# Optimization experiments

Measured on AMD Instinct MI355X. Metric: run time of the kernel, lower is better.

Reference implementation:

```python
import jax, jax.numpy as jnp
import numpy as np

B, S, HID = 1, 4096, 2304
NH, NKV, HD = 8, 4, 256
SLIDING_WINDOW = 2048
SOFTCAP = 50.0
SCALE = 256.0 ** -0.5  # query_pre_attn_scalar ** -0.5
ROPE_THETA = 10000.0
MASK_MIN = -1e9


def setup_inputs() -> dict:
    key = jax.random.key(0)
    k1, k2, k3 = jax.random.split(key, 3)
    hidden_states = jax.random.normal(k1, (B, S, HID), dtype=jnp.float32)
    position_ids = jnp.arange(S, dtype=jnp.int64)[None, :]
    # causal + sliding-window additive mask [B,1,S,S]
    i = jnp.arange(S)[:, None]
    j = jnp.arange(S)[None, :]
    allowed = (j <= i) & (j > i - SLIDING_WINDOW)
    attention_mask = jnp.where(allowed, 0.0, MASK_MIN).astype(jnp.float32)[None, None]
    Wqkv = jax.random.normal(k2, ((NH + 2 * NKV) * HD, HID), dtype=jnp.float32) * 0.02
    Wo = jax.random.normal(k3, (HID, NH * HD), dtype=jnp.float32) * 0.02
    return {"hidden_states": hidden_states, "attention_mask": attention_mask,
            "position_ids": position_ids, "Wqkv": Wqkv, "Wo": Wo}


def _rotate_half(x):
    x1, x2 = jnp.split(x, 2, axis=-1)
    return jnp.concatenate([-x2, x1], axis=-1)


def _rope(position_ids):
    inv_freq = 1.0 / (ROPE_THETA ** (jnp.arange(0, HD, 2, dtype=jnp.float32) / HD))
    freqs = position_ids.astype(jnp.float32)[..., None] * inv_freq[None, None, :]  # [B,S,HD/2]
    emb = jnp.concatenate([freqs, freqs], axis=-1)  # [B,S,HD]
    return jnp.cos(emb), jnp.sin(emb)


def reference(hidden_states, attention_mask, position_ids, Wqkv, Wo):
    bsz, q_len, _ = hidden_states.shape
    qkv = hidden_states @ Wqkv.T  # [B,S,(NH+2*NKV)*HD]
    q, k, v = jnp.split(qkv, [NH * HD, (NH + NKV) * HD], axis=-1)
    q = q.reshape(bsz, q_len, NH, HD).transpose(0, 2, 1, 3)   # [B,NH,S,HD]
    k = k.reshape(bsz, q_len, NKV, HD).transpose(0, 2, 1, 3)  # [B,NKV,S,HD]
    v = v.reshape(bsz, q_len, NKV, HD).transpose(0, 2, 1, 3)

    cos, sin = _rope(position_ids)          # [B,S,HD]
    cos, sin = cos[:, None], sin[:, None]   # [B,1,S,HD]
    q = q * cos + _rotate_half(q) * sin
    k = k * cos + _rotate_half(k) * sin

    # repeat_kv for GQA
    groups = NH // NKV
    k = jnp.repeat(k, groups, axis=1)  # [B,NH,S,HD]
    v = jnp.repeat(v, groups, axis=1)

    attn = jnp.einsum('bhqd,bhkd->bhqk', q, k) * SCALE
    attn = jnp.tanh(attn / SOFTCAP) * SOFTCAP  # logit softcapping
    attn = attn + attention_mask[:, :, :, :q_len]
    attn = jax.nn.softmax(attn.astype(jnp.float32), axis=-1).astype(q.dtype)
    out = jnp.einsum('bhqk,bhkd->bhqd', attn, v)
    out = out.transpose(0, 2, 1, 3).reshape(bsz, q_len, NH * HD)
    return out @ Wo.T  # [B,S,HID]
```

## Files before the change

kernel.cpp:

```cpp
#include <hip/hip_runtime.h>

typedef unsigned short u16;
typedef unsigned int u32;
typedef __attribute__((ext_vector_type(8))) __bf16 bf16x8;
typedef __attribute__((ext_vector_type(4))) float f32x4;

#define SLEN 4096
#define HIDDEN 2304
#define NHEADS 8
#define NKVH 4
#define HDIM 256
#define WINDOW 2048

__device__ __forceinline__ u16 f2b(float x) {
  u32 u = __float_as_uint(x);
  u32 r = (u + 0x7fffu + ((u >> 16) & 1u)) >> 16;
  return (u16)r;
}

__device__ __forceinline__ void load_lds16(const void* g, void* l) {
  __builtin_amdgcn_global_load_lds((const __attribute__((address_space(1))) u32*)g,
                                   (__attribute__((address_space(3))) u32*)l,
                                   16, 0, 0);
}

__global__ __launch_bounds__(256) void k_f2b(const float* __restrict__ in,
                                             u16* __restrict__ out, int n4) {
  int i = blockIdx.x * 256 + threadIdx.x;
  if (i >= n4) return;
  float4 v = ((const float4*)in)[i];
  ushort4 o;
  o.x = f2b(v.x); o.y = f2b(v.y); o.z = f2b(v.z); o.w = f2b(v.w);
  ((ushort4*)out)[i] = o;
}

template<int M, int N, int K>
__global__ __launch_bounds__(256) void gemm_bt(const u16* __restrict__ A,
                                               const u16* __restrict__ B,
                                               float* __restrict__ C) {
  constexpr int NTN = N / 128;
  __shared__ u16 As[128 * 32];
  __shared__ u16 Bs[128 * 32];
  const int tid = threadIdx.x;
  const int lane = tid & 63;
  const int w = tid >> 6;
  const int wr = (w >> 1) * 64, wc = (w & 1) * 64;
  const int l15 = lane & 15, l4 = lane >> 4;
  const size_t m0 = (size_t)(blockIdx.x / NTN) * 128;
  const size_t n0 = (size_t)(blockIdx.x % NTN) * 128;
  const int r = tid >> 2;
  const int cbe = (tid & 3) * 8;
  const u16* Ag = A + (m0 + r) * K + cbe;
  const u16* Bg = B + (n0 + r) * K + cbe;
  char* Asb = (char*)As + w * 1024;
  char* Bsb = (char*)Bs + w * 1024;
  f32x4 acc[4][4];
#pragma unroll
  for (int i = 0; i < 4; ++i)
#pragma unroll
    for (int j = 0; j < 4; ++j) { f32x4 z = {0.f, 0.f, 0.f, 0.f}; acc[i][j] = z; }

  for (int kt = 0; kt < K; kt += 32) {
    load_lds16(Ag + kt, Asb);
    load_lds16(Ag + kt + (size_t)64 * K, Asb + 4096);
    load_lds16(Bg + kt, Bsb);
    load_lds16(Bg + kt + (size_t)64 * K, Bsb + 4096);
    __syncthreads();
    bf16x8 a[4], b[4];
#pragma unroll
    for (int mi = 0; mi < 4; ++mi)
      a[mi] = *(const bf16x8*)&As[(wr + mi * 16 + l15) * 32 + l4 * 8];
#pragma unroll
    for (int ni = 0; ni < 4; ++ni)
      b[ni] = *(const bf16x8*)&Bs[(wc + ni * 16 + l15) * 32 + l4 * 8];
#pragma unroll
    for (int mi = 0; mi < 4; ++mi)
#pragma unroll
      for (int ni = 0; ni < 4; ++ni)
        acc[mi][ni] = __builtin_amdgcn_mfma_f32_16x16x32_bf16(a[mi], b[ni], acc[mi][ni], 0, 0, 0);
    __syncthreads();
  }
#pragma unroll
  for (int mi = 0; mi < 4; ++mi) {
#pragma unroll
    for (int ni = 0; ni < 4; ++ni) {
      size_t row = m0 + wr + mi * 16 + l4 * 4;
      size_t col = n0 + wc + ni * 16 + l15;
      float* Cp = C + row * N + col;
#pragma unroll
      for (int j = 0; j < 4; ++j) Cp[(size_t)j * N] = acc[mi][ni][j];
    }
  }
}

__global__ __launch_bounds__(256) void k_rope(const float* __restrict__ qkv,
                                              u16* __restrict__ Qb, u16* __restrict__ Kb,
                                              u16* __restrict__ Vb) {
  const int s = blockIdx.x;
  const float* row = qkv + (size_t)s * 4096;
  const float pos = (float)s;
  const int tid = threadIdx.x;
  for (int idx = tid; idx < 1536; idx += 256) {
    int h = idx >> 7;
    int d = idx & 127;
    float inv = expf((float)d * -0.07195578415987644f);
    float ang = pos * inv;
    float sn, c;
    sincosf(ang, &sn, &c);
    int colbase = (h < 8) ? (h << 8) : (2048 + ((h - 8) << 8));
    float x1 = row[colbase + d];
    float x2 = row[colbase + d + 128];
    float o1 = x1 * c - x2 * sn;
    float o2 = x2 * c + x1 * sn;
    u16* dst = (h < 8) ? (Qb + ((size_t)h * SLEN + s) * HDIM)
                       : (Kb + ((size_t)(h - 8) * SLEN + s) * HDIM);
    dst[d] = f2b(o1);
    dst[d + 128] = f2b(o2);
  }
  for (int idx = tid; idx < 1024; idx += 256) {
    int h = idx >> 8;
    int d = idx & 255;
    Vb[((size_t)h * SLEN + s) * HDIM + d] = f2b(row[3072 + idx]);
  }
}

__global__ __launch_bounds__(256) void k_attn(const u16* __restrict__ Qb,
                                              const u16* __restrict__ Kb,
                                              const u16* __restrict__ Vb,
                                              u16* __restrict__ AO) {
  __shared__ char kbuf[32768];
  __shared__ char vbuf[36864];
  __shared__ char pbuf[8192];
  const int tid = threadIdx.x;
  const int lane = tid & 63;
  const int w = tid >> 6;
  const int l15 = lane & 15, l4 = lane >> 4;
  const int h = blockIdx.y;
  const int q0 = blockIdx.x * 64;
  const u16* Qh = Qb + (size_t)h * SLEN * HDIM;
  const u16* Kh = Kb + (size_t)(h >> 1) * SLEN * HDIM;
  const u16* Vh = Vb + (size_t)(h >> 1) * SLEN * HDIM;

  bf16x8 qa[8];
  {
    const u16* qrow = Qh + (size_t)(q0 + w * 16 + l15) * HDIM + l4 * 8;
#pragma unroll
    for (int ks = 0; ks < 8; ++ks) qa[ks] = *(const bf16x8*)(qrow + ks * 32);
  }
  f32x4 O[16];
#pragma unroll
  for (int i = 0; i < 16; ++i) { f32x4 z = {0.f, 0.f, 0.f, 0.f}; O[i] = z; }
  float mrow[4] = {-50.f, -50.f, -50.f, -50.f};
  float lrow[4] = {0.f, 0.f, 0.f, 0.f};

  const int t_lo = (q0 >= WINDOW) ? ((q0 - (WINDOW - 1)) >> 6) : 0;
  const int t_hi = q0 >> 6;
  for (int t = t_lo; t <= t_hi; ++t) {
    const int k0 = t * 64;
#pragma unroll
    for (int p = 0; p < 8; ++p) {
      int b = (p * 256 + tid) * 16;
      int g = b ^ (((b >> 9) & 7) << 4);
      load_lds16((const char*)Kh + (size_t)k0 * 512 + g, kbuf + p * 4096 + w * 1024);
    }
#pragma unroll
    for (int p = 0; p < 8; ++p) {
      int chunk = p * 256 + tid;
      int krow = chunk >> 5;
      int d0 = (chunk & 31) * 8;
      uint4 vv = *(const uint4*)((const char*)Vh + (size_t)(k0 + krow) * 512 + d0 * 2);
      u32 mv[4] = {vv.x, vv.y, vv.z, vv.w};
      u32 ov[4];
      ov[0] = (u32)__shfl_xor((int)vv.x, 32);
      ov[1] = (u32)__shfl_xor((int)vv.y, 32);
      ov[2] = (u32)__shfl_xor((int)vv.z, 32);
      ov[3] = (u32)__shfl_xor((int)vv.w, 32);
      int kk = krow & ~1;
      int dsh = ((d0 >> 3) & 7) << 4;
      if (lane < 32) {
#pragma unroll
        for (int jj = 0; jj < 4; ++jj) {
          u32 me = (mv[jj >> 1] >> (16 * (jj & 1))) & 0xffffu;
          u32 ot = (ov[jj >> 1] >> (16 * (jj & 1))) & 0xffffu;
          int a = ((d0 + jj) * 144 + kk * 2) ^ dsh;
          *(u32*)(vbuf + a) = me | (ot << 16);
        }
      } else {
#pragma unroll
        for (int jj = 4; jj < 8; ++jj) {
          u32 me = (mv[jj >> 1] >> (16 * (jj & 1))) & 0xffffu;
          u32 ot = (ov[jj >> 1] >> (16 * (jj & 1))) & 0xffffu;
          int a = ((d0 + jj) * 144 + kk * 2) ^ dsh;
          *(u32*)(vbuf + a) = ot | (me << 16);
        }
      }
    }
    __syncthreads();

    f32x4 sc[4];
#pragma unroll
    for (int n = 0; n < 4; ++n) { f32x4 z = {0.f, 0.f, 0.f, 0.f}; sc[n] = z; }
#pragma unroll
    for (int ks = 0; ks < 8; ++ks) {
#pragma unroll
      for (int n = 0; n < 4; ++n) {
        int row = n * 16 + l15;
        int a = (row * 512 + ks * 64 + l4 * 16) ^ ((row & 7) << 4);
        bf16x8 kb = *(const bf16x8*)(kbuf + a);
        sc[n] = __builtin_amdgcn_mfma_f32_16x16x32_bf16(qa[ks], kb, sc[n], 0, 0, 0);
      }
    }
    const bool need_mask = (k0 + 63 > q0) || (k0 < q0 - 1984);
    const int i_base = q0 + w * 16 + l4 * 4;
    const int k_base = k0 + l15;
    float rmax[4] = {-1e30f, -1e30f, -1e30f, -1e30f};
#pragma unroll
    for (int n = 0; n < 4; ++n) {
#pragma unroll
      for (int j = 0; j < 4; ++j) {
        float t2 = __expf(sc[n][j] * 0.0025f);
        float y = 50.f - 100.f / (t2 + 1.f);
        if (need_mask) {
          int ig = i_base + j;
          int kg = k_base + n * 16;
          if (kg > ig || kg < ig - (WINDOW - 1)) y = -1e9f;
        }
        sc[n][j] = y;
        rmax[j] = fmaxf(rmax[j], y);
      }
    }
#pragma unroll
    for (int j = 0; j < 4; ++j) {
      rmax[j] = fmaxf(rmax[j], __shfl_xor(rmax[j], 1));
      rmax[j] = fmaxf(rmax[j], __shfl_xor(rmax[j], 2));
      rmax[j] = fmaxf(rmax[j], __shfl_xor(rmax[j], 4));
      rmax[j] = fmaxf(rmax[j], __shfl_xor(rmax[j], 8));
    }
    f32x4 ev;
    float pm[4];
#pragma unroll
    for (int j = 0; j < 4; ++j) {
      float mn = fmaxf(mrow[j], rmax[j]);
      ev[j] = __expf(mrow[j] - mn);
      mrow[j] = mn;
      pm[j] = mn;
    }
    float rsum[4] = {0.f, 0.f, 0.f, 0.f};
#pragma unroll
    for (int n = 0; n < 4; ++n)
#pragma unroll
      for (int j = 0; j < 4; ++j) {
        float pv = __expf(sc[n][j] - pm[j]);
        sc[n][j] = pv;
        rsum[j] += pv;
      }
#pragma unroll
    for (int j = 0; j < 4; ++j) {
      rsum[j] += __shfl_xor(rsum[j], 1);
      rsum[j] += __shfl_xor(rsum[j], 2);
      rsum[j] += __shfl_xor(rsum[j], 4);
      rsum[j] += __shfl_xor(rsum[j], 8);
      lrow[j] = lrow[j] * ev[j] + rsum[j];
    }
#pragma unroll
    for (int i = 0; i < 16; ++i) O[i] *= ev;

#pragma unroll
    for (int n = 0; n < 4; ++n)
#pragma unroll
      for (int j = 0; j < 4; ++j) {
        int prow = l4 * 4 + j;
        int a = (prow * 128 + (n * 16 + l15) * 2) ^ ((prow & 7) << 4);
        *(u16*)(pbuf + w * 2048 + a) = f2b(sc[n][j]);
      }
#pragma unroll
    for (int ks2 = 0; ks2 < 2; ++ks2) {
      int a = (l15 * 128 + ks2 * 64 + l4 * 16) ^ ((l15 & 7) << 4);
      bf16x8 pa = *(const bf16x8*)(pbuf + w * 2048 + a);
#pragma unroll
      for (int nn = 0; nn < 16; ++nn) {
        int d = nn * 16 + l15;
        int va = (d * 144 + ks2 * 64 + l4 * 16) ^ (((d >> 3) & 7) << 4);
        bf16x8 vb2 = *(const bf16x8*)(vbuf + va);
        O[nn] = __builtin_amdgcn_mfma_f32_16x16x32_bf16(pa, vb2, O[nn], 0, 0, 0);
      }
    }
    __syncthreads();
  }
  f32x4 linv;
#pragma unroll
  for (int j = 0; j < 4; ++j) linv[j] = 1.f / lrow[j];
  const size_t orow = (size_t)(q0 + w * 16 + l4 * 4);
#pragma unroll
  for (int nn = 0; nn < 16; ++nn) {
    f32x4 o = O[nn] * linv;
#pragma unroll
    for (int j = 0; j < 4; ++j)
      AO[(orow + j) * 2048 + h * 256 + nn * 16 + l15] = f2b(o[j]);
  }
}

extern "C" void kernel_launch(void* const* d_in, const int* in_sizes, int n_in,
                              void* d_out, int out_size, void* d_ws, size_t ws_size,
                              hipStream_t stream) {
  (void)in_sizes; (void)n_in; (void)out_size; (void)ws_size;
  const float* hidden = (const float*)d_in[0];
  const float* Wqkv = (const float*)d_in[3];
  const float* Wo = (const float*)d_in[4];

  char* base = (char*)d_ws;
  const size_t SZ_HID = (size_t)SLEN * HIDDEN * 2;
  const size_t SZ_WQKV = (size_t)4096 * HIDDEN * 2;
  const size_t SZ_WO = (size_t)HIDDEN * 2048 * 2;
  const size_t SZ_Q = (size_t)NHEADS * SLEN * HDIM * 2;
  const size_t SZ_K = (size_t)NKVH * SLEN * HDIM * 2;

  u16* hid_b = (u16*)base;
  u16* wqkv_b = (u16*)(base + SZ_HID);
  u16* wo_b = (u16*)(base + SZ_HID + SZ_WQKV);
  float* qkv = (float*)(base + SZ_HID + SZ_WQKV + SZ_WO);
  u16* Qv = (u16*)base;
  u16* Kv = (u16*)(base + SZ_Q);
  u16* Vv = (u16*)(base + SZ_Q + SZ_K);
  u16* AO = (u16*)qkv;

  k_f2b<<<SLEN * HIDDEN / 4 / 256, 256, 0, stream>>>(hidden, hid_b, SLEN * HIDDEN / 4);
  k_f2b<<<4096 * HIDDEN / 4 / 256, 256, 0, stream>>>(Wqkv, wqkv_b, 4096 * HIDDEN / 4);
  k_f2b<<<HIDDEN * 2048 / 4 / 256, 256, 0, stream>>>(Wo, wo_b, HIDDEN * 2048 / 4);

  gemm_bt<4096, 4096, 2304><<<dim3(32 * 32), 256, 0, stream>>>(hid_b, wqkv_b, qkv);
  k_rope<<<SLEN, 256, 0, stream>>>(qkv, Qv, Kv, Vv);
  k_attn<<<dim3(64, 8), 256, 0, stream>>>(Qv, Kv, Vv, AO);
  gemm_bt<4096, 2304, 2048><<<dim3(32 * 18), 256, 0, stream>>>(AO, wo_b, (float*)d_out);
}
```

Measured before the change: 841.9 us.

## Pre-transpose V and read K/V directly from global in single-wave attention blocks

Adds a separate kernel that writes V transposed (head, dim, seq) in bf16, so the PV MFMA operand can be loaded straight from global memory. The attention kernel becomes one 64-thread wave per 16-query tile. It drops the shared-memory staging of K and V and the block-wide barriers, relying on L1/L2 caching for reuse. The goal is more blocks in flight and no synchronisation, at the cost of losing K/V sharing across four waves, so global and cache traffic per query rises.

```diff
diff --git a/kernel.cpp b/kernel.cpp
--- a/kernel.cpp
+++ b/kernel.cpp
@@ -94,8 +94,7 @@
 }
 
 __global__ __launch_bounds__(256) void k_rope(const float* __restrict__ qkv,
-                                              u16* __restrict__ Qb, u16* __restrict__ Kb,
-                                              u16* __restrict__ Vb) {
+                                              u16* __restrict__ Qb, u16* __restrict__ Kb) {
   const int s = blockIdx.x;
   const float* row = qkv + (size_t)s * 4096;
   const float pos = (float)s;
@@ -117,33 +116,56 @@
     dst[d] = f2b(o1);
     dst[d + 128] = f2b(o2);
   }
-  for (int idx = tid; idx < 1024; idx += 256) {
-    int h = idx >> 8;
-    int d = idx & 255;
-    Vb[((size_t)h * SLEN + s) * HDIM + d] = f2b(row[3072 + idx]);
-  }
-}
-
-__global__ __launch_bounds__(256) void k_attn(const u16* __restrict__ Qb,
-                                              const u16* __restrict__ Kb,
-                                              const u16* __restrict__ Vb,
-                                              u16* __restrict__ AO) {
-  __shared__ char kbuf[32768];
-  __shared__ char vbuf[36864];
-  __shared__ char pbuf[8192];
+}
+
+__global__ __launch_bounds__(256) void k_vt(const float* __restrict__ qkv,
+                                            u16* __restrict__ Vt) {
+  __shared__ u16 t[64][272];
   const int tid = threadIdx.x;
-  const int lane = tid & 63;
-  const int w = tid >> 6;
+  const int h = blockIdx.y;
+  const int s0 = blockIdx.x * 64;
+#pragma unroll
+  for (int pass = 0; pass < 16; ++pass) {
+    int r = pass * 4 + (tid >> 6);
+    int c4 = (tid & 63) * 4;
+    float4 v = *(const float4*)(qkv + (size_t)(s0 + r) * 4096 + 3072 + h * 256 + c4);
+    t[r][c4] = f2b(v.x); t[r][c4 + 1] = f2b(v.y);
+    t[r][c4 + 2] = f2b(v.z); t[r][c4 + 3] = f2b(v.w);
+  }
+  __syncthreads();
+#pragma unroll
+  for (int i = 0; i < 8; ++i) {
+    int chunk = i * 256 + tid;
+    int d = chunk >> 3;
+    int s8 = (chunk & 7) * 8;
+    u16 tmp[8];
+#pragma unroll
+    for (int j = 0; j < 8; ++j) tmp[j] = t[s8 + j][d];
+    uint4 o;
+    o.x = (u32)tmp[0] | ((u32)tmp[1] << 16);
+    o.y = (u32)tmp[2] | ((u32)tmp[3] << 16);
+    o.z = (u32)tmp[4] | ((u32)tmp[5] << 16);
+    o.w = (u32)tmp[6] | ((u32)tmp[7] << 16);
+    *(uint4*)(Vt + ((size_t)h * HDIM + d) * SLEN + s0 + s8) = o;
+  }
+}
+
+__global__ __launch_bounds__(64, 2) void k_attn(const u16* __restrict__ Qb,
+                                                const u16* __restrict__ Kb,
+                                                const u16* __restrict__ Vt,
+                                                u16* __restrict__ AO) {
+  __shared__ char pbuf[2048];
+  const int lane = threadIdx.x & 63;
   const int l15 = lane & 15, l4 = lane >> 4;
   const int h = blockIdx.y;
-  const int q0 = blockIdx.x * 64;
+  const int q0 = blockIdx.x * 16;
   const u16* Qh = Qb + (size_t)h * SLEN * HDIM;
   const u16* Kh = Kb + (size_t)(h >> 1) * SLEN * HDIM;
-  const u16* Vh = Vb + (size_t)(h >> 1) * SLEN * HDIM;
+  const u16* Vth = Vt + (size_t)(h >> 1) * HDIM * SLEN;
 
   bf16x8 qa[8];
   {
-    const u16* qrow = Qh + (size_t)(q0 + w * 16 + l15) * HDIM + l4 * 8;
+    const u16* qrow = Qh + (size_t)(q0 + l15) * HDIM + l4 * 8;
 #pragma unroll
     for (int ks = 0; ks < 8; ++ks) qa[ks] = *(const bf16x8*)(qrow + ks * 32);
   }
@@ -157,46 +179,6 @@
   const int t_hi = q0 >> 6;
   for (int t = t_lo; t <= t_hi; ++t) {
     const int k0 = t * 64;
-#pragma unroll
-    for (int p = 0; p < 8; ++p) {
-      int b = (p * 256 + tid) * 16;
-      int g = b ^ (((b >> 9) & 7) << 4);
-      load_lds16((const char*)Kh + (size_t)k0 * 512 + g, kbuf + p * 4096 + w * 1024);
-    }
-#pragma unroll
-    for (int p = 0; p < 8; ++p) {
-      int chunk = p * 256 + tid;
-      int krow = chunk >> 5;
-      int d0 = (chunk & 31) * 8;
-      uint4 vv = *(const uint4*)((const char*)Vh + (size_t)(k0 + krow) * 512 + d0 * 2);
-      u32 mv[4] = {vv.x, vv.y, vv.z, vv.w};
-      u32 ov[4];
-      ov[0] = (u32)__shfl_xor((int)vv.x, 32);
-      ov[1] = (u32)__shfl_xor((int)vv.y, 32);
-      ov[2] = (u32)__shfl_xor((int)vv.z, 32);
-      ov[3] = (u32)__shfl_xor((int)vv.w, 32);
-      int kk = krow & ~1;
-      int dsh = ((d0 >> 3) & 7) << 4;
-      if (lane < 32) {
-#pragma unroll
-        for (int jj = 0; jj < 4; ++jj) {
-          u32 me = (mv[jj >> 1] >> (16 * (jj & 1))) & 0xffffu;
-          u32 ot = (ov[jj >> 1] >> (16 * (jj & 1))) & 0xffffu;
-          int a = ((d0 + jj) * 144 + kk * 2) ^ dsh;
-          *(u32*)(vbuf + a) = me | (ot << 16);
-        }
-      } else {
-#pragma unroll
-        for (int jj = 4; jj < 8; ++jj) {
-          u32 me = (mv[jj >> 1] >> (16 * (jj & 1))) & 0xffffu;
-          u32 ot = (ov[jj >> 1] >> (16 * (jj & 1))) & 0xffffu;
-          int a = ((d0 + jj) * 144 + kk * 2) ^ dsh;
-          *(u32*)(vbuf + a) = ot | (me << 16);
-        }
-      }
-    }
-    __syncthreads();
-
     f32x4 sc[4];
 #pragma unroll
     for (int n = 0; n < 4; ++n) { f32x4 z = {0.f, 0.f, 0.f, 0.f}; sc[n] = z; }
@@ -204,14 +186,12 @@
     for (int ks = 0; ks < 8; ++ks) {
 #pragma unroll
       for (int n = 0; n < 4; ++n) {
-        int row = n * 16 + l15;
-        int a = (row * 512 + ks * 64 + l4 * 16) ^ ((row & 7) << 4);
-        bf16x8 kb = *(const bf16x8*)(kbuf + a);
+        bf16x8 kb = *(const bf16x8*)(Kh + (size_t)(k0 + n * 16 + l15) * HDIM + ks * 32 + l4 * 8);
         sc[n] = __builtin_amdgcn_mfma_f32_16x16x32_bf16(qa[ks], kb, sc[n], 0, 0, 0);
       }
     }
-    const bool need_mask = (k0 + 63 > q0) || (k0 < q0 - 1984);
-    const int i_base = q0 + w * 16 + l4 * 4;
+    const bool need_mask = (k0 + 63 > q0) || (k0 < q0 - 2032);
+    const int i_base = q0 + l4 * 4;
     const int k_base = k0 + l15;
     float rmax[4] = {-1e30f, -1e30f, -1e30f, -1e30f};
 #pragma unroll
@@ -271,26 +251,23 @@
       for (int j = 0; j < 4; ++j) {
         int prow = l4 * 4 + j;
         int a = (prow * 128 + (n * 16 + l15) * 2) ^ ((prow & 7) << 4);
-        *(u16*)(pbuf + w * 2048 + a) = f2b(sc[n][j]);
+        *(u16*)(pbuf + a) = f2b(sc[n][j]);
       }
 #pragma unroll
     for (int ks2 = 0; ks2 < 2; ++ks2) {
       int a = (l15 * 128 + ks2 * 64 + l4 * 16) ^ ((l15 & 7) << 4);
-      bf16x8 pa = *(const bf16x8*)(pbuf + w * 2048 + a);
+      bf16x8 pa = *(const bf16x8*)(pbuf + a);
 #pragma unroll
       for (int nn = 0; nn < 16; ++nn) {
-        int d = nn * 16 + l15;
-        int va = (d * 144 + ks2 * 64 + l4 * 16) ^ (((d >> 3) & 7) << 4);
-        bf16x8 vb2 = *(const bf16x8*)(vbuf + va);
-        O[nn] = __builtin_amdgcn_mfma_f32_16x16x32_bf16(pa, vb2, O[nn], 0, 0, 0);
-      }
-    }
-    __syncthreads();
+        bf16x8 vb = *(const bf16x8*)(Vth + (size_t)(nn * 16 + l15) * SLEN + k0 + ks2 * 32 + l4 * 8);
+        O[nn] = __builtin_amdgcn_mfma_f32_16x16x32_bf16(pa, vb, O[nn], 0, 0, 0);
+      }
+    }
   }
   f32x4 linv;
 #pragma unroll
   for (int j = 0; j < 4; ++j) linv[j] = 1.f / lrow[j];
-  const size_t orow = (size_t)(q0 + w * 16 + l4 * 4);
+  const size_t orow = (size_t)(q0 + l4 * 4);
 #pragma unroll
   for (int nn = 0; nn < 16; ++nn) {
     f32x4 o = O[nn] * linv;
@@ -321,7 +298,7 @@
   float* qkv = (float*)(base + SZ_HID + SZ_WQKV + SZ_WO);
   u16* Qv = (u16*)base;
   u16* Kv = (u16*)(base + SZ_Q);
-  u16* Vv = (u16*)(base + SZ_Q + SZ_K);
+  u16* Vt = (u16*)(base + SZ_Q + SZ_K);
   u16* AO = (u16*)qkv;
 
   k_f2b<<<SLEN * HIDDEN / 4 / 256, 256, 0, stream>>>(hidden, hid_b, SLEN * HIDDEN / 4);
@@ -329,7 +306,8 @@
   k_f2b<<<HIDDEN * 2048 / 4 / 256, 256, 0, stream>>>(Wo, wo_b, HIDDEN * 2048 / 4);
 
   gemm_bt<4096, 4096, 2304><<<dim3(32 * 32), 256, 0, stream>>>(hid_b, wqkv_b, qkv);
-  k_rope<<<SLEN, 256, 0, stream>>>(qkv, Qv, Kv, Vv);
-  k_attn<<<dim3(64, 8), 256, 0, stream>>>(Qv, Kv, Vv, AO);
+  k_rope<<<SLEN, 256, 0, stream>>>(qkv, Qv, Kv);
+  k_vt<<<dim3(64, NKVH), 256, 0, stream>>>(qkv, Vt);
+  k_attn<<<dim3(256, NHEADS), 64, 0, stream>>>(Qv, Kv, Vt, AO);
   gemm_bt<4096, 2304, 2048><<<dim3(32 * 18), 256, 0, stream>>>(AO, wo_b, (float*)d_out);
 }
```

New measurement: 945.0 us. 1.12x slower.
